# Kernel optimization log

Hardware: AMD Instinct MI355X
Metric: run time of the kernel (lower is better)

## Reference

```python
import jax, jax.numpy as jnp
import numpy as np

N = 100000
E = 1600000
IN_C = 256
HID = 256
OUT_C = 32
K = 2          # APPNP K = max(1, num_layers)
ALPHA = 0.1


def setup_inputs() -> dict:
    key = jax.random.key(0)
    ks = jax.random.split(key, 8)
    x = jax.random.normal(ks[0], (N, IN_C), dtype=jnp.float32)
    edge_index = jax.random.randint(ks[1], (2, E), 0, N, dtype=jnp.int64)
    s_in = 1.0 / np.sqrt(IN_C)
    s_h = 1.0 / np.sqrt(HID)
    W_in = jax.random.uniform(ks[2], (IN_C, HID), jnp.float32, -s_in, s_in)
    b_in = jax.random.uniform(ks[3], (HID,), jnp.float32, -s_in, s_in)
    W_h = jax.random.uniform(ks[4], (HID, HID), jnp.float32, -s_h, s_h)
    b_h = jax.random.uniform(ks[5], (HID,), jnp.float32, -s_h, s_h)
    W_out = jax.random.uniform(ks[6], (HID, OUT_C), jnp.float32, -s_h, s_h)
    b_out = jax.random.uniform(ks[7], (OUT_C,), jnp.float32, -s_h, s_h)
    return {"x": x, "edge_index": edge_index, "W_in": W_in, "b_in": b_in,
            "W_h": W_h, "b_h": b_h, "W_out": W_out, "b_out": b_out}


def _appnp(h0, src, dst):
    # gcn_norm with added self-loops: deg over destinations, sym normalization
    loops = jnp.arange(N, dtype=src.dtype)
    src_f = jnp.concatenate([src, loops])  # [E+N]
    dst_f = jnp.concatenate([dst, loops])
    deg = jax.ops.segment_sum(jnp.ones_like(dst_f, dtype=h0.dtype), dst_f,
                              num_segments=N)
    dinv = jnp.where(deg > 0, jax.lax.rsqrt(jnp.maximum(deg, 1e-12)), 0.0)
    norm = (dinv[src_f] * dinv[dst_f])[:, None]  # [E+N, 1]
    h = h0
    for _ in range(K):
        agg = jax.ops.segment_sum(h[src_f] * norm, dst_f, num_segments=N)
        h = (1.0 - ALPHA) * agg + ALPHA * h0
    return h


def reference(x, edge_index, W_in, b_in, W_h, b_h, W_out, b_out):
    # MLP encoder (dropout inactive in eval mode)
    h = jax.nn.relu(x @ W_in + b_in)
    h = jax.nn.relu(h @ W_h + b_h)
    h = h @ W_out + b_out  # [N, OUT_C]
    return _appnp(h, edge_index[0], edge_index[1])
```

## Files before the change

kernel.cpp:

```cpp
#include <hip/hip_runtime.h>

#define NN 100000
#define NE 1600000
#define NTILE 3125

#define BSH 7
#define BNODES 128
#define NBUCK 782
#define NBUCKP 784
#define CAP 2560
#define ECH 8192
#define NCHK 196
#define WFRAG_BLKS 272

typedef _Float16 half8v __attribute__((ext_vector_type(8)));
typedef _Float16 half4v __attribute__((ext_vector_type(4)));
typedef float f32x4 __attribute__((ext_vector_type(4)));


__device__ __forceinline__ void wfrag_one(const float* __restrict__ W,
                                          _Float16* __restrict__ Wf, int idx, int N) {
    int j = idx & 7;
    int l = (idx >> 3) & 63;
    int f = idx >> 9;
    int nt = f % (N / 16);
    int kt = f / (N / 16);
    int k = kt * 32 + (l >> 4) * 8 + j;
    int c = nt * 16 + (l & 15);
    Wf[idx] = (_Float16)W[k * N + c];
}


__global__ __launch_bounds__(512) void k_count_wfrag(const int* __restrict__ dst,
                                                     int* __restrict__ histT,
                                                     const float* __restrict__ W1,
                                                     const float* __restrict__ W2,
                                                     const float* __restrict__ W3,
                                                     _Float16* __restrict__ Wf1,
                                                     _Float16* __restrict__ Wf2,
                                                     _Float16* __restrict__ Wf3) {
    const int t = threadIdx.x;
    if (blockIdx.x >= NCHK) {
        int idx = (blockIdx.x - NCHK) * 512 + t;
        if (idx < 65536) wfrag_one(W1, Wf1, idx, 256);
        else if (idx < 131072) wfrag_one(W2, Wf2, idx - 65536, 256);
        else if (idx < 139264) wfrag_one(W3, Wf3, idx - 131072, 32);
        return;
    }
    __shared__ int h[NBUCKP];
    const int blk = blockIdx.x;
    for (int b = t; b < NBUCKP; b += 512) h[b] = 0;
    __syncthreads();
    const int ebase = blk * ECH + t * 16;
#pragma unroll
    for (int q = 0; q < 4; q++) {
        int e = ebase + q * 4;
        if (e + 4 <= NE) {
            int4 d4 = *reinterpret_cast<const int4*>(dst + e);
            atomicAdd(&h[d4.x >> BSH], 1);
            atomicAdd(&h[d4.y >> BSH], 1);
            atomicAdd(&h[d4.z >> BSH], 1);
            atomicAdd(&h[d4.w >> BSH], 1);
        } else {
            for (int p = e; p < NE; p++) atomicAdd(&h[dst[p] >> BSH], 1);
            break;
        }
    }
    __syncthreads();
    for (int b = t; b < NBUCK; b += 512) histT[(long long)b * NCHK + blk] = h[b];
}


__global__ __launch_bounds__(256) void k_scanb(int* __restrict__ histT,
                                               int* __restrict__ cntb) {
    __shared__ int s[256];
    const int b = blockIdx.x, t = threadIdx.x;
    int* row = histT + (long long)b * NCHK;
    int v = (t < NCHK) ? row[t] : 0;
    s[t] = v;
    __syncthreads();
    for (int off = 1; off < 256; off <<= 1) {
        int u = (t >= off) ? s[t - off] : 0;
        __syncthreads();
        s[t] += u;
        __syncthreads();
    }
    if (t < NCHK) row[t] = s[t] - v;
    if (t == 255) cntb[b] = s[255];
}


__global__ __launch_bounds__(512) void k_part_lay1(const int* __restrict__ src,
                                                   const int* __restrict__ dst,
                                                   const int* __restrict__ histT,
                                                   int* __restrict__ data,
                                                   const float* __restrict__ x,
                                                   const _Float16* __restrict__ Wf1,
                                                   const float* __restrict__ b1,
                                                   _Float16* __restrict__ h1g) {
    __shared__ char smem[16384];
    const int t = threadIdx.x;

    if (blockIdx.x < NCHK) {
        int* curs = (int*)smem;
        const int blk = blockIdx.x;
        for (int b = t; b < NBUCKP; b += 512)
            curs[b] = b * CAP + ((b < NBUCK) ? histT[(long long)b * NCHK + blk] : 0);
        __syncthreads();
        const int ebase = blk * ECH + t * 16;
#pragma unroll
        for (int q = 0; q < 4; q++) {
            int e = ebase + q * 4;
            if (e + 4 <= NE) {
                int4 d4 = *reinterpret_cast<const int4*>(dst + e);
                int4 s4 = *reinterpret_cast<const int4*>(src + e);
                int p0 = atomicAdd(&curs[d4.x >> BSH], 1);
                data[p0] = (s4.x << BSH) | (d4.x & (BNODES - 1));
                int p1 = atomicAdd(&curs[d4.y >> BSH], 1);
                data[p1] = (s4.y << BSH) | (d4.y & (BNODES - 1));
                int p2 = atomicAdd(&curs[d4.z >> BSH], 1);
                data[p2] = (s4.z << BSH) | (d4.z & (BNODES - 1));
                int p3 = atomicAdd(&curs[d4.w >> BSH], 1);
                data[p3] = (s4.w << BSH) | (d4.w & (BNODES - 1));
            } else {
                for (int p = e; p < NE; p++) {
                    int d = dst[p], sv = src[p];
                    int pos = atomicAdd(&curs[d >> BSH], 1);
                    data[pos] = (sv << BSH) | (d & (BNODES - 1));
                }
                break;
            }
        }
        return;
    }

    char* buf = smem;
    const int lane = t & 63;
    const int G = lane >> 4;
    const int w = t >> 6;
    const int T = blockIdx.x - NCHK;

    half8v wr[8][2];
    {
        const half8v* W1f = reinterpret_cast<const half8v*>(Wf1);
#pragma unroll
        for (int kt = 0; kt < 8; kt++)
#pragma unroll
            for (int n2 = 0; n2 < 2; n2++)
                wr[kt][n2] = W1f[(kt * 16 + 2 * w + n2) * 64 + lane];
    }
    float bvs[2];
#pragma unroll
    for (int n2 = 0; n2 < 2; n2++) bvs[n2] = b1[w * 32 + n2 * 16 + (lane & 15)];

    {
        const float4* A4 = reinterpret_cast<const float4*>(x + (size_t)T * 32 * 256);
#pragma unroll
        for (int i = t; i < 2048; i += 512) {
            int r = i >> 6, c4 = i & 63;
            float4 v = A4[i];
            half4v hv;
            hv[0] = (_Float16)v.x; hv[1] = (_Float16)v.y;
            hv[2] = (_Float16)v.z; hv[3] = (_Float16)v.w;
            int bo = (r * 512 + c4 * 8) ^ ((r & 7) << 4);
            *reinterpret_cast<half4v*>(buf + bo) = hv;
        }
    }
    __syncthreads();

    f32x4 acc[2][2];
#pragma unroll
    for (int mt = 0; mt < 2; mt++)
#pragma unroll
        for (int n2 = 0; n2 < 2; n2++) acc[mt][n2] = (f32x4)0.f;
#pragma unroll
    for (int kt = 0; kt < 8; kt++) {
        half8v a[2];
#pragma unroll
        for (int mt = 0; mt < 2; mt++) {
            int row = mt * 16 + (lane & 15);
            int bo = (row * 512 + kt * 64 + (G << 4)) ^ ((row & 7) << 4);
            a[mt] = *reinterpret_cast<const half8v*>(buf + bo);
        }
#pragma unroll
        for (int mt = 0; mt < 2; mt++)
#pragma unroll
            for (int n2 = 0; n2 < 2; n2++)
                acc[mt][n2] = __builtin_amdgcn_mfma_f32_16x16x32_f16(a[mt], wr[kt][n2], acc[mt][n2], 0, 0, 0);
    }
    __syncthreads();

#pragma unroll
    for (int mt = 0; mt < 2; mt++)
#pragma unroll
        for (int n2 = 0; n2 < 2; n2++) {
            int colc = w * 32 + n2 * 16 + (lane & 15);
            float bb = bvs[n2];
#pragma unroll
            for (int r = 0; r < 4; r++) {
                int row = mt * 16 + G * 4 + r;
                float v = fmaxf(acc[mt][n2][r] + bb, 0.f);
                int bo = (row * 512 + colc * 2) ^ ((row & 7) << 4);
                *reinterpret_cast<_Float16*>(buf + bo) = (_Float16)v;
            }
        }
    __syncthreads();

    {
        half8v* dstp = reinterpret_cast<half8v*>(h1g + (size_t)T * 8192);
        const half8v* srcp = reinterpret_cast<const half8v*>(buf);
#pragma unroll
        for (int i = t; i < 1024; i += 512) dstp[i] = srcp[i];
    }
}


__global__ __launch_bounds__(256) void k_sortb(const int* __restrict__ data,
                                               const int* __restrict__ cntb,
                                               int* __restrict__ col,
                                               int* __restrict__ begp,
                                               int* __restrict__ endp,
                                               float* __restrict__ dinv) {
    __shared__ int hist[BNODES];
    __shared__ int scn[BNODES];
    __shared__ int curs[BNODES];
    const int b = blockIdx.x, t = threadIdx.x;
    if (t < BNODES) hist[t] = 0;
    __syncthreads();
    const int cnt = cntb[b];
    const int* wp = data + b * CAP;
    for (int e = t; e < cnt; e += 256) atomicAdd(&hist[wp[e] & (BNODES - 1)], 1);
    __syncthreads();
    if (t < BNODES) scn[t] = hist[t];
    __syncthreads();
    for (int off = 1; off < BNODES; off <<= 1) {
        int v = (t < BNODES && t >= off) ? scn[t - off] : 0;
        __syncthreads();
        if (t < BNODES) scn[t] += v;
        __syncthreads();
    }
    if (t < BNODES) {
        int beg = scn[t] - hist[t];
        curs[t] = beg;
        int node = (b << BSH) + t;
        if (node < NN) {
            begp[node] = b * CAP + beg;
            endp[node] = b * CAP + scn[t];
            dinv[node] = rsqrtf((float)(hist[t] + 1));
        }
    }
    __syncthreads();
    for (int e = t; e < cnt; e += 256) {
        int w = wp[e];
        int p = atomicAdd(&curs[w & (BNODES - 1)], 1);
        col[b * CAP + p] = w >> BSH;
    }
}


__global__ __launch_bounds__(512) void k_lay23(const _Float16* __restrict__ h1g,
                                               const _Float16* __restrict__ Wf2,
                                               const _Float16* __restrict__ Wf3,
                                               const float* __restrict__ b2,
                                               const float* __restrict__ b3,
                                               const float* __restrict__ dinv,
                                               _Float16* __restrict__ h0f,
                                               _Float16* __restrict__ hs0) {
    __shared__ char buf[32 * 512];
    const int t = threadIdx.x;
    const int lane = t & 63;
    const int G = lane >> 4;
    const int w = t >> 6;
    const int T = blockIdx.x;

    half8v wr[8][2];
    {
        const half8v* W2f = reinterpret_cast<const half8v*>(Wf2);
#pragma unroll
        for (int kt = 0; kt < 8; kt++)
#pragma unroll
            for (int n2 = 0; n2 < 2; n2++)
                wr[kt][n2] = W2f[(kt * 16 + 2 * w + n2) * 64 + lane];
    }
    float bvs[2];
#pragma unroll
    for (int n2 = 0; n2 < 2; n2++) bvs[n2] = b2[w * 32 + n2 * 16 + (lane & 15)];

    {
        const half8v* srcp = reinterpret_cast<const half8v*>(h1g + (size_t)T * 8192);
        half8v* dstp = reinterpret_cast<half8v*>(buf);
#pragma unroll
        for (int i = t; i < 1024; i += 512) dstp[i] = srcp[i];
    }
    __syncthreads();

    f32x4 acc[2][2];
#pragma unroll
    for (int mt = 0; mt < 2; mt++)
#pragma unroll
        for (int n2 = 0; n2 < 2; n2++) acc[mt][n2] = (f32x4)0.f;
#pragma unroll
    for (int kt = 0; kt < 8; kt++) {
        half8v a[2];
#pragma unroll
        for (int mt = 0; mt < 2; mt++) {
            int row = mt * 16 + (lane & 15);
            int bo = (row * 512 + kt * 64 + (G << 4)) ^ ((row & 7) << 4);
            a[mt] = *reinterpret_cast<const half8v*>(buf + bo);
        }
#pragma unroll
        for (int mt = 0; mt < 2; mt++)
#pragma unroll
            for (int n2 = 0; n2 < 2; n2++)
                acc[mt][n2] = __builtin_amdgcn_mfma_f32_16x16x32_f16(a[mt], wr[kt][n2], acc[mt][n2], 0, 0, 0);
    }
    __syncthreads();

#pragma unroll
    for (int mt = 0; mt < 2; mt++)
#pragma unroll
        for (int n2 = 0; n2 < 2; n2++) {
            int colc = w * 32 + n2 * 16 + (lane & 15);
            float bb = bvs[n2];
#pragma unroll
            for (int r = 0; r < 4; r++) {
                int row = mt * 16 + G * 4 + r;
                float v = fmaxf(acc[mt][n2][r] + bb, 0.f);
                int bo = (row * 512 + colc * 2) ^ ((row & 7) << 4);
                *reinterpret_cast<_Float16*>(buf + bo) = (_Float16)v;
            }
        }
    __syncthreads();

    if (w < 4) {
        const half8v* W3f = reinterpret_cast<const half8v*>(Wf3);
        const int mt3 = w >> 1, ct3 = w & 1;
        const float bb3 = b3[ct3 * 16 + (lane & 15)];
        f32x4 a3 = (f32x4)0.f;
#pragma unroll
        for (int kt = 0; kt < 8; kt++) {
            int row = mt3 * 16 + (lane & 15);
            int bo = (row * 512 + kt * 64 + (G << 4)) ^ ((row & 7) << 4);
            half8v a = *reinterpret_cast<const half8v*>(buf + bo);
            half8v b = W3f[(kt * 2 + ct3) * 64 + lane];
            a3 = __builtin_amdgcn_mfma_f32_16x16x32_f16(a, b, a3, 0, 0, 0);
        }
        int colc = ct3 * 16 + (lane & 15);
#pragma unroll
        for (int r = 0; r < 4; r++) {
            size_t row = (size_t)T * 32 + mt3 * 16 + G * 4 + r;
            float v = a3[r] + bb3;
            h0f[row * 32 + colc] = (_Float16)v;
            hs0[row * 32 + colc] = (_Float16)(dinv[row] * v);
        }
    }
}


template<bool FINAL>
__global__ __launch_bounds__(256) void k_appnp(const int* __restrict__ begp,
                                               const int* __restrict__ endp,
                                               const int* __restrict__ col,
                                               const float* __restrict__ dinv,
                                               const _Float16* __restrict__ hs,
                                               const _Float16* __restrict__ h0f,
                                               void* __restrict__ outp) {
    int node = blockIdx.x * 4 + (threadIdx.x >> 6);
    if (node >= NN) return;
    const int lane = threadIdx.x & 63;
    const int slot = lane >> 2;
    const int cg = lane & 3;

    const int beg = begp[node];
    const int end = endp[node];
    const float dd = dinv[node];
    const half8v selfv = *reinterpret_cast<const half8v*>(hs + (size_t)node * 32 + cg * 8);
    const half8v h0v = *reinterpret_cast<const half8v*>(h0f + (size_t)node * 32 + cg * 8);

    float acc[8];
#pragma unroll
    for (int j = 0; j < 8; j++) acc[j] = 0.f;

    for (int e = beg + slot; e < end; e += 16) {
        int s = col[e];
        half8v v = *reinterpret_cast<const half8v*>(hs + (size_t)s * 32 + cg * 8);
#pragma unroll
        for (int j = 0; j < 8; j++) acc[j] += (float)v[j];
    }

#pragma unroll
    for (int off = 4; off < 64; off <<= 1) {
#pragma unroll
        for (int j = 0; j < 8; j++) acc[j] += __shfl_xor(acc[j], off, 64);
    }

    if (slot == 0) {
        float o[8];
#pragma unroll
        for (int j = 0; j < 8; j++)
            o[j] = 0.9f * dd * (acc[j] + (float)selfv[j]) + 0.1f * (float)h0v[j];
        size_t off = (size_t)node * 32 + cg * 8;
        if (FINAL) {
            float4 v0 = make_float4(o[0], o[1], o[2], o[3]);
            float4 v1 = make_float4(o[4], o[5], o[6], o[7]);
            float4* op = reinterpret_cast<float4*>((float*)outp + off);
            op[0] = v0; op[1] = v1;
        } else {
            half8v hv;
#pragma unroll
            for (int j = 0; j < 8; j++) hv[j] = (_Float16)(dd * o[j]);
            *reinterpret_cast<half8v*>((_Float16*)outp + off) = hv;
        }
    }
}


extern "C" void kernel_launch(void* const* d_in, const int* in_sizes, int n_in,
                              void* d_out, int out_size, void* d_ws, size_t ws_size,
                              hipStream_t stream) {
    const float* x     = (const float*)d_in[0];
    const int*   ei    = (const int*)d_in[1];
    const float* W_in  = (const float*)d_in[2];
    const float* b_in  = (const float*)d_in[3];
    const float* W_h   = (const float*)d_in[4];
    const float* b_h   = (const float*)d_in[5];
    const float* W_out = (const float*)d_in[6];
    const float* b_out = (const float*)d_in[7];
    float* out = (float*)d_out;

    const int* srcv = ei;
    const int* dstv = ei + NE;

    char* ws = (char*)d_ws;
    _Float16* h0f  = (_Float16*)ws;
    _Float16* hs0  = h0f + (size_t)NN * 32;
    _Float16* hs1  = hs0 + (size_t)NN * 32;
    float* dinv    = (float*)(hs1 + (size_t)NN * 32);
    _Float16* Wf_in  = (_Float16*)(dinv + NN);
    _Float16* Wf_h   = Wf_in + 256 * 256;
    _Float16* Wf_out = Wf_h + 256 * 256;
    _Float16* h1g    = Wf_out + 256 * 32;
    int* histT = (int*)(h1g + (size_t)NN * 256);
    int* cntb  = histT + (size_t)NBUCK * NCHK;
    int* data  = cntb + NBUCKP;
    int* col   = data + (size_t)NBUCKP * CAP;
    int* begp  = col + (size_t)NBUCKP * CAP;
    int* endp  = begp + NN;

    k_count_wfrag<<<NCHK + WFRAG_BLKS, 512, 0, stream>>>(dstv, histT,
                                                         W_in, W_h, W_out,
                                                         Wf_in, Wf_h, Wf_out);
    k_scanb<<<NBUCK, 256, 0, stream>>>(histT, cntb);

    k_part_lay1<<<NCHK + NTILE, 512, 0, stream>>>(srcv, dstv, histT, data,
                                                  x, Wf_in, b_in, h1g);

    k_sortb<<<NBUCK, 256, 0, stream>>>(data, cntb, col, begp, endp, dinv);

    k_lay23<<<NTILE, 512, 0, stream>>>(h1g, Wf_h, Wf_out, b_h, b_out, dinv, h0f, hs0);

    k_appnp<false><<<(NN + 3) / 4, 256, 0, stream>>>(begp, endp, col, dinv, hs0, h0f, hs1);
    k_appnp<true ><<<(NN + 3) / 4, 256, 0, stream>>>(begp, endp, col, dinv, hs1, h0f, out);
}
```

Before: 166.1 us.

## Split partition from layer-1 GEMM and enlarge MLP row tiles to 64

```diff
diff --git a/kernel.cpp b/kernel.cpp
--- a/kernel.cpp
+++ b/kernel.cpp
@@ -2,7 +2,7 @@
 
 #define NN 100000
 #define NE 1600000
-#define NTILE 3125
+#define NT64 1563
 
 #define BSH 7
 #define BNODES 128
@@ -90,75 +90,66 @@
 }
 
 
-__global__ __launch_bounds__(512) void k_part_lay1(const int* __restrict__ src,
-                                                   const int* __restrict__ dst,
-                                                   const int* __restrict__ histT,
-                                                   int* __restrict__ data,
-                                                   const float* __restrict__ x,
-                                                   const _Float16* __restrict__ Wf1,
-                                                   const float* __restrict__ b1,
-                                                   _Float16* __restrict__ h1g) {
-    __shared__ char smem[16384];
+__global__ __launch_bounds__(512) void k_part(const int* __restrict__ src,
+                                              const int* __restrict__ dst,
+                                              const int* __restrict__ histT,
+                                              int* __restrict__ data) {
+    __shared__ int curs[NBUCKP];
+    const int t = threadIdx.x, blk = blockIdx.x;
+    for (int b = t; b < NBUCKP; b += 512)
+        curs[b] = b * CAP + ((b < NBUCK) ? histT[(long long)b * NCHK + blk] : 0);
+    __syncthreads();
+    const int ebase = blk * ECH + t * 16;
+#pragma unroll
+    for (int q = 0; q < 4; q++) {
+        int e = ebase + q * 4;
+        if (e + 4 <= NE) {
+            int4 d4 = *reinterpret_cast<const int4*>(dst + e);
+            int4 s4 = *reinterpret_cast<const int4*>(src + e);
+            int p0 = atomicAdd(&curs[d4.x >> BSH], 1);
+            data[p0] = (s4.x << BSH) | (d4.x & (BNODES - 1));
+            int p1 = atomicAdd(&curs[d4.y >> BSH], 1);
+            data[p1] = (s4.y << BSH) | (d4.y & (BNODES - 1));
+            int p2 = atomicAdd(&curs[d4.z >> BSH], 1);
+            data[p2] = (s4.z << BSH) | (d4.z & (BNODES - 1));
+            int p3 = atomicAdd(&curs[d4.w >> BSH], 1);
+            data[p3] = (s4.w << BSH) | (d4.w & (BNODES - 1));
+        } else {
+            for (int p = e; p < NE; p++) {
+                int d = dst[p], sv = src[p];
+                int pos = atomicAdd(&curs[d >> BSH], 1);
+                data[pos] = (sv << BSH) | (d & (BNODES - 1));
+            }
+            break;
+        }
+    }
+}
+
+
+__global__ __launch_bounds__(512) void k_lay1(const float* __restrict__ x,
+                                              const _Float16* __restrict__ Wf1,
+                                              const float* __restrict__ b1,
+                                              _Float16* __restrict__ h1g) {
+    __shared__ char buf[64 * 512];
     const int t = threadIdx.x;
-
-    if (blockIdx.x < NCHK) {
-        int* curs = (int*)smem;
-        const int blk = blockIdx.x;
-        for (int b = t; b < NBUCKP; b += 512)
-            curs[b] = b * CAP + ((b < NBUCK) ? histT[(long long)b * NCHK + blk] : 0);
-        __syncthreads();
-        const int ebase = blk * ECH + t * 16;
-#pragma unroll
-        for (int q = 0; q < 4; q++) {
-            int e = ebase + q * 4;
-            if (e + 4 <= NE) {
-                int4 d4 = *reinterpret_cast<const int4*>(dst + e);
-                int4 s4 = *reinterpret_cast<const int4*>(src + e);
-                int p0 = atomicAdd(&curs[d4.x >> BSH], 1);
-                data[p0] = (s4.x << BSH) | (d4.x & (BNODES - 1));
-                int p1 = atomicAdd(&curs[d4.y >> BSH], 1);
-                data[p1] = (s4.y << BSH) | (d4.y & (BNODES - 1));
-                int p2 = atomicAdd(&curs[d4.z >> BSH], 1);
-                data[p2] = (s4.z << BSH) | (d4.z & (BNODES - 1));
-                int p3 = atomicAdd(&curs[d4.w >> BSH], 1);
-                data[p3] = (s4.w << BSH) | (d4.w & (BNODES - 1));
-            } else {
-                for (int p = e; p < NE; p++) {
-                    int d = dst[p], sv = src[p];
-                    int pos = atomicAdd(&curs[d >> BSH], 1);
-                    data[pos] = (sv << BSH) | (d & (BNODES - 1));
-                }
-                break;
-            }
-        }
-        return;
-    }
-
-    char* buf = smem;
     const int lane = t & 63;
     const int G = lane >> 4;
     const int w = t >> 6;
-    const int T = blockIdx.x - NCHK;
-
-    half8v wr[8][2];
+    const int T = blockIdx.x;
+    const long long row0 = (long long)T * 64;
+
+    const half8v* W1f = reinterpret_cast<const half8v*>(Wf1);
+    float bvs[2];
+#pragma unroll
+    for (int n2 = 0; n2 < 2; n2++) bvs[n2] = b1[w * 32 + n2 * 16 + (lane & 15)];
+
     {
-        const half8v* W1f = reinterpret_cast<const half8v*>(Wf1);
-#pragma unroll
-        for (int kt = 0; kt < 8; kt++)
-#pragma unroll
-            for (int n2 = 0; n2 < 2; n2++)
-                wr[kt][n2] = W1f[(kt * 16 + 2 * w + n2) * 64 + lane];
-    }
-    float bvs[2];
-#pragma unroll
-    for (int n2 = 0; n2 < 2; n2++) bvs[n2] = b1[w * 32 + n2 * 16 + (lane & 15)];
-
-    {
-        const float4* A4 = reinterpret_cast<const float4*>(x + (size_t)T * 32 * 256);
-#pragma unroll
-        for (int i = t; i < 2048; i += 512) {
+        const float4* A4 = reinterpret_cast<const float4*>(x + row0 * 256);
+#pragma unroll
+        for (int i = t; i < 4096; i += 512) {
             int r = i >> 6, c4 = i & 63;
-            float4 v = A4[i];
+            float4 v = make_float4(0.f, 0.f, 0.f, 0.f);
+            if (row0 + r < NN) v = A4[i];
             half4v hv;
             hv[0] = (_Float16)v.x; hv[1] = (_Float16)v.y;
             hv[2] = (_Float16)v.z; hv[3] = (_Float16)v.w;
@@ -168,30 +159,33 @@
     }
     __syncthreads();
 
-    f32x4 acc[2][2];
-#pragma unroll
-    for (int mt = 0; mt < 2; mt++)
+    f32x4 acc[4][2];
+#pragma unroll
+    for (int mt = 0; mt < 4; mt++)
 #pragma unroll
         for (int n2 = 0; n2 < 2; n2++) acc[mt][n2] = (f32x4)0.f;
 #pragma unroll
     for (int kt = 0; kt < 8; kt++) {
-        half8v a[2];
-#pragma unroll
-        for (int mt = 0; mt < 2; mt++) {
+        half8v a[4], bfr[2];
+#pragma unroll
+        for (int n2 = 0; n2 < 2; n2++)
+            bfr[n2] = W1f[(kt * 16 + 2 * w + n2) * 64 + lane];
+#pragma unroll
+        for (int mt = 0; mt < 4; mt++) {
             int row = mt * 16 + (lane & 15);
             int bo = (row * 512 + kt * 64 + (G << 4)) ^ ((row & 7) << 4);
             a[mt] = *reinterpret_cast<const half8v*>(buf + bo);
         }
 #pragma unroll
-        for (int mt = 0; mt < 2; mt++)
+        for (int mt = 0; mt < 4; mt++)
 #pragma unroll
             for (int n2 = 0; n2 < 2; n2++)
-                acc[mt][n2] = __builtin_amdgcn_mfma_f32_16x16x32_f16(a[mt], wr[kt][n2], acc[mt][n2], 0, 0, 0);
-    }
-    __syncthreads();
-
-#pragma unroll
-    for (int mt = 0; mt < 2; mt++)
+                acc[mt][n2] = __builtin_amdgcn_mfma_f32_16x16x32_f16(a[mt], bfr[n2], acc[mt][n2], 0, 0, 0);
+    }
+    __syncthreads();
+
+#pragma unroll
+    for (int mt = 0; mt < 4; mt++)
 #pragma unroll
         for (int n2 = 0; n2 < 2; n2++) {
             int colc = w * 32 + n2 * 16 + (lane & 15);
@@ -207,10 +201,10 @@
     __syncthreads();
 
     {
-        half8v* dstp = reinterpret_cast<half8v*>(h1g + (size_t)T * 8192);
+        half8v* dstp = reinterpret_cast<half8v*>(h1g + (size_t)T * 16384);
         const half8v* srcp = reinterpret_cast<const half8v*>(buf);
 #pragma unroll
-        for (int i = t; i < 1024; i += 512) dstp[i] = srcp[i];
+        for (int i = t; i < 2048; i += 512) dstp[i] = srcp[i];
     }
 }
 
@@ -266,58 +260,54 @@
                                                const float* __restrict__ dinv,
                                                _Float16* __restrict__ h0f,
                                                _Float16* __restrict__ hs0) {
-    __shared__ char buf[32 * 512];
+    __shared__ char buf[64 * 512];
     const int t = threadIdx.x;
     const int lane = t & 63;
     const int G = lane >> 4;
     const int w = t >> 6;
     const int T = blockIdx.x;
-
-    half8v wr[8][2];
+    const long long row0 = (long long)T * 64;
+
+    const half8v* W2f = reinterpret_cast<const half8v*>(Wf2);
+    float bvs[2];
+#pragma unroll
+    for (int n2 = 0; n2 < 2; n2++) bvs[n2] = b2[w * 32 + n2 * 16 + (lane & 15)];
+
     {
-        const half8v* W2f = reinterpret_cast<const half8v*>(Wf2);
-#pragma unroll
-        for (int kt = 0; kt < 8; kt++)
-#pragma unroll
-            for (int n2 = 0; n2 < 2; n2++)
-                wr[kt][n2] = W2f[(kt * 16 + 2 * w + n2) * 64 + lane];
-    }
-    float bvs[2];
-#pragma unroll
-    for (int n2 = 0; n2 < 2; n2++) bvs[n2] = b2[w * 32 + n2 * 16 + (lane & 15)];
-
-    {
-        const half8v* srcp = reinterpret_cast<const half8v*>(h1g + (size_t)T * 8192);
+        const half8v* srcp = reinterpret_cast<const half8v*>(h1g + (size_t)T * 16384);
         half8v* dstp = reinterpret_cast<half8v*>(buf);
 #pragma unroll
-        for (int i = t; i < 1024; i += 512) dstp[i] = srcp[i];
-    }
-    __syncthreads();
-
-    f32x4 acc[2][2];
-#pragma unroll
-    for (int mt = 0; mt < 2; mt++)
+        for (int i = t; i < 2048; i += 512) dstp[i] = srcp[i];
+    }
+    __syncthreads();
+
+    f32x4 acc[4][2];
+#pragma unroll
+    for (int mt = 0; mt < 4; mt++)
 #pragma unroll
         for (int n2 = 0; n2 < 2; n2++) acc[mt][n2] = (f32x4)0.f;
 #pragma unroll
     for (int kt = 0; kt < 8; kt++) {
-        half8v a[2];
-#pragma unroll
-        for (int mt = 0; mt < 2; mt++) {
+        half8v a[4], bfr[2];
+#pragma unroll
+        for (int n2 = 0; n2 < 2; n2++)
+            bfr[n2] = W2f[(kt * 16 + 2 * w + n2) * 64 + lane];
+#pragma unroll
+        for (int mt = 0; mt < 4; mt++) {
             int row = mt * 16 + (lane & 15);
             int bo = (row * 512 + kt * 64 + (G << 4)) ^ ((row & 7) << 4);
             a[mt] = *reinterpret_cast<const half8v*>(buf + bo);
         }
 #pragma unroll
-        for (int mt = 0; mt < 2; mt++)
+        for (int mt = 0; mt < 4; mt++)
 #pragma unroll
             for (int n2 = 0; n2 < 2; n2++)
-                acc[mt][n2] = __builtin_amdgcn_mfma_f32_16x16x32_f16(a[mt], wr[kt][n2], acc[mt][n2], 0, 0, 0);
-    }
-    __syncthreads();
-
-#pragma unroll
-    for (int mt = 0; mt < 2; mt++)
+                acc[mt][n2] = __builtin_amdgcn_mfma_f32_16x16x32_f16(a[mt], bfr[n2], acc[mt][n2], 0, 0, 0);
+    }
+    __syncthreads();
+
+#pragma unroll
+    for (int mt = 0; mt < 4; mt++)
 #pragma unroll
         for (int n2 = 0; n2 < 2; n2++) {
             int colc = w * 32 + n2 * 16 + (lane & 15);
@@ -332,7 +322,7 @@
         }
     __syncthreads();
 
-    if (w < 4) {
+    {
         const half8v* W3f = reinterpret_cast<const half8v*>(Wf3);
         const int mt3 = w >> 1, ct3 = w & 1;
         const float bb3 = b3[ct3 * 16 + (lane & 15)];
@@ -348,10 +338,12 @@
         int colc = ct3 * 16 + (lane & 15);
 #pragma unroll
         for (int r = 0; r < 4; r++) {
-            size_t row = (size_t)T * 32 + mt3 * 16 + G * 4 + r;
-            float v = a3[r] + bb3;
-            h0f[row * 32 + colc] = (_Float16)v;
-            hs0[row * 32 + colc] = (_Float16)(dinv[row] * v);
+            long long row = row0 + mt3 * 16 + G * 4 + r;
+            if (row < NN) {
+                float v = a3[r] + bb3;
+                h0f[row * 32 + colc] = (_Float16)v;
+                hs0[row * 32 + colc] = (_Float16)(dinv[row] * v);
+            }
         }
     }
 }
@@ -440,7 +432,7 @@
     _Float16* Wf_h   = Wf_in + 256 * 256;
     _Float16* Wf_out = Wf_h + 256 * 256;
     _Float16* h1g    = Wf_out + 256 * 32;
-    int* histT = (int*)(h1g + (size_t)NN * 256);
+    int* histT = (int*)(h1g + (size_t)NT64 * 16384);
     int* cntb  = histT + (size_t)NBUCK * NCHK;
     int* data  = cntb + NBUCKP;
     int* col   = data + (size_t)NBUCKP * CAP;
@@ -452,12 +444,13 @@
                                                          Wf_in, Wf_h, Wf_out);
     k_scanb<<<NBUCK, 256, 0, stream>>>(histT, cntb);
 
-    k_part_lay1<<<NCHK + NTILE, 512, 0, stream>>>(srcv, dstv, histT, data,
-                                                  x, Wf_in, b_in, h1g);
+    k_part<<<NCHK, 512, 0, stream>>>(srcv, dstv, histT, data);
+
+    k_lay1<<<NT64, 512, 0, stream>>>(x, Wf_in, b_in, h1g);
 
     k_sortb<<<NBUCK, 256, 0, stream>>>(data, cntb, col, begp, endp, dinv);
 
-    k_lay23<<<NTILE, 512, 0, stream>>>(h1g, Wf_h, Wf_out, b_h, b_out, dinv, h0f, hs0);
+    k_lay23<<<NT64, 512, 0, stream>>>(h1g, Wf_h, Wf_out, b_h, b_out, dinv, h0f, hs0);
 
     k_appnp<false><<<(NN + 3) / 4, 256, 0, stream>>>(begp, endp, col, dinv, hs0, h0f, hs1);
     k_appnp<true ><<<(NN + 3) / 4, 256, 0, stream>>>(begp, endp, col, dinv, hs1, h0f, out);
```

After: 172.2 us. +3.7%, slower.
